# Performance work log

Measured on AMD Instinct MI355X. Metric: run time of the kernel, lower is better.

Reference implementation:

```python
import jax, jax.numpy as jnp
import numpy as np

E = 500_000
NODE_DIM = 128
EDGE_DIM = 128
GLOB_DIM = 64
NUM_GRAPHS = 64
HIDDEN = 4 * EDGE_DIM  # 512
IN_DIM = 2 * NODE_DIM + EDGE_DIM + GLOB_DIM  # 448
EPS = 1e-5


def setup_inputs() -> dict:
    key = jax.random.key(0)
    ks = jax.random.split(key, 12)
    src = jax.random.normal(ks[0], (E, NODE_DIM), dtype=jnp.float32)
    dest = jax.random.normal(ks[1], (E, NODE_DIM), dtype=jnp.float32)
    edge_attr = jax.random.normal(ks[2], (E, EDGE_DIM), dtype=jnp.float32)
    u = jax.random.normal(ks[3], (NUM_GRAPHS, GLOB_DIM), dtype=jnp.float32)
    batch = jnp.sort(jax.random.randint(ks[4], (E,), 0, NUM_GRAPHS, dtype=jnp.int32))
    # MLP params (kaiming-ish scale)
    W1 = jax.random.normal(ks[5], (IN_DIM, HIDDEN), dtype=jnp.float32) / np.sqrt(IN_DIM)
    b1 = jnp.zeros((HIDDEN,), dtype=jnp.float32)
    W2 = jax.random.normal(ks[6], (HIDDEN, EDGE_DIM), dtype=jnp.float32) / np.sqrt(HIDDEN)
    b2 = jnp.zeros((EDGE_DIM,), dtype=jnp.float32)
    # GraphNorm params
    gn_weight = jnp.ones((EDGE_DIM,), dtype=jnp.float32)
    gn_bias = jnp.zeros((EDGE_DIM,), dtype=jnp.float32)
    mean_scale = jnp.ones((EDGE_DIM,), dtype=jnp.float32)
    return {"src": src, "dest": dest, "edge_attr": edge_attr, "u": u, "batch": batch,
            "W1": W1, "b1": b1, "W2": W2, "b2": b2,
            "gn_weight": gn_weight, "gn_bias": gn_bias, "mean_scale": mean_scale}


def _graph_norm(x, batch, weight, bias, mean_scale):
    # per-graph mean
    cnt = jax.ops.segment_sum(jnp.ones((x.shape[0],), x.dtype), batch, num_segments=NUM_GRAPHS)
    cnt = jnp.maximum(cnt, 1.0)[:, None]  # [G,1]
    mean = jax.ops.segment_sum(x, batch, num_segments=NUM_GRAPHS) / cnt  # [G,D]
    out = x - mean[batch] * mean_scale
    var = jax.ops.segment_sum(out * out, batch, num_segments=NUM_GRAPHS) / cnt  # [G,D]
    std = jnp.sqrt(var + EPS)
    return out / std[batch] * weight + bias


def reference(src, dest, edge_attr, u, batch, W1, b1, W2, b2, gn_weight, gn_bias, mean_scale):
    # gather per-graph globals + concat: [E, 2*node+edge+glob]
    h = jnp.concatenate([src, dest, edge_attr, u[batch]], axis=1)
    h = jax.nn.relu(h @ W1 + b1) @ W2 + b2  # [E, edge_dim]
    out = _graph_norm(h + edge_attr, batch, gn_weight, gn_bias, mean_scale)
    return out  # dropout is identity in eval / p=0.0
```

## Files before the change

kernel.cpp:

```cpp
#include <hip/hip_runtime.h>
#include <stdint.h>

#define E_EDGES   500000
#define MBLK      32
#define NBLK      15625
#define EPSV      1e-5f

typedef unsigned short u16;
typedef __attribute__((ext_vector_type(8))) short short8;
typedef __attribute__((ext_vector_type(4))) float f32x4;

__device__ __forceinline__ u16 f2bf(float f) {
  uint32_t u = __float_as_uint(f);
  u += 0x7fffu + ((u >> 16) & 1u);
  return (u16)(u >> 16);
}

__global__ void prep_weights(const float* __restrict__ W1, const float* __restrict__ W2,
                             u16* __restrict__ w1f, u16* __restrict__ w2f) {
  int idx = blockIdx.x * blockDim.x + threadIdx.x;
  if (idx < 32*14*64) {
    int lane = idx & 63; int t = idx >> 6; int k32 = t % 14; int n16 = t / 14;
    int n = n16*16 + (lane & 15); int k0 = k32*32 + (lane >> 4)*8;
    short8 pk;
#pragma unroll
    for (int j = 0; j < 8; ++j) pk[j] = (short)f2bf(W1[(size_t)(k0 + j)*512 + n]);
    *(short8*)&w1f[(size_t)idx * 8] = pk;
  } else if (idx < 32*14*64 + 8*16*64) {
    int i2 = idx - 32*14*64;
    int lane = i2 & 63; int t = i2 >> 6; int k32 = t % 16; int n16 = t / 16;
    int n = n16*16 + (lane & 15); int k0 = k32*32 + (lane >> 4)*8;
    short8 pk;
#pragma unroll
    for (int j = 0; j < 8; ++j) pk[j] = (short)f2bf(W2[(size_t)(k0 + j)*128 + n]);
    *(short8*)&w2f[(size_t)i2 * 8] = pk;
  }
}

#define SWZ16(row, byte) ((byte) ^ (((row) & 7) << 4))

__global__ __launch_bounds__(256, 4)
void fused_kernel(const float* __restrict__ srcp, const float* __restrict__ destp,
                  const float* __restrict__ edgep, const float* __restrict__ up,
                  const int* __restrict__ batch, const float* __restrict__ b1,
                  const float* __restrict__ b2,
                  const u16* __restrict__ w1f, const u16* __restrict__ w2f,
                  float* __restrict__ outp,
                  float* __restrict__ sums0, float* __restrict__ sums2,
                  float* __restrict__ cntsh, int nshard) {
  const int tid  = threadIdx.x;
  const int lane = tid & 63;
  const int w    = tid >> 6;
  const int l15  = lane & 15, l4 = lane >> 4;

  __shared__ __align__(16) u16 lds[32*512];
  char* ldsb = (char*)lds;

  const long grow0 = (long)blockIdx.x * MBLK;

  {
    const int srow = tid >> 3;
    const int c8   = (tid & 7) * 8;
    const long sgrow = grow0 + srow;
    const int  bat = batch[sgrow];
#pragma unroll
    for (int j = 0; j < 7; ++j) {
      const float* sp;
      if (j == 0)      sp = srcp  + sgrow*128 + c8;
      else if (j == 1) sp = srcp  + sgrow*128 + 64 + c8;
      else if (j == 2) sp = destp + sgrow*128 + c8;
      else if (j == 3) sp = destp + sgrow*128 + 64 + c8;
      else if (j == 4) sp = edgep + sgrow*128 + c8;
      else if (j == 5) sp = edgep + sgrow*128 + 64 + c8;
      else             sp = up + (size_t)bat*64 + c8;
      f32x4 t0 = *(const f32x4*)(sp);
      f32x4 t1 = *(const f32x4*)(sp + 4);
      short8 pk;
      pk[0]=(short)f2bf(t0[0]); pk[1]=(short)f2bf(t0[1]);
      pk[2]=(short)f2bf(t0[2]); pk[3]=(short)f2bf(t0[3]);
      pk[4]=(short)f2bf(t1[0]); pk[5]=(short)f2bf(t1[1]);
      pk[6]=(short)f2bf(t1[2]); pk[7]=(short)f2bf(t1[3]);
      *(short8*)(ldsb + srow*896 + SWZ16(srow, (j*64 + c8)*2)) = pk;
    }
  }
  __syncthreads();

  f32x4 acc1[2][8];
#pragma unroll
  for (int mi = 0; mi < 2; ++mi)
#pragma unroll
    for (int nj = 0; nj < 8; ++nj) {
      float bv = b1[w*128 + nj*16 + l15];
      acc1[mi][nj] = (f32x4){bv, bv, bv, bv};
    }

#pragma unroll 2
  for (int k32 = 0; k32 < 14; ++k32) {
    short8 a[2], b[8];
#pragma unroll
    for (int mi = 0; mi < 2; ++mi) {
      int row = mi*16 + l15;
      a[mi] = *(const short8*)(ldsb + row*896 + SWZ16(row, k32*64 + l4*16));
    }
#pragma unroll
    for (int nj = 0; nj < 8; ++nj) {
      int n16 = w*8 + nj;
      b[nj] = *(const short8*)&w1f[((size_t)(n16*14 + k32)*64 + lane)*8];
    }
#pragma unroll
    for (int mi = 0; mi < 2; ++mi)
#pragma unroll
      for (int nj = 0; nj < 8; ++nj)
        acc1[mi][nj] = __builtin_amdgcn_mfma_f32_16x16x32_bf16(a[mi], b[nj], acc1[mi][nj], 0, 0, 0);
  }
  __syncthreads();

#pragma unroll
  for (int nj = 0; nj < 8; ++nj) {
    int n = w*128 + nj*16 + l15;
#pragma unroll
    for (int mi = 0; mi < 2; ++mi)
#pragma unroll
      for (int rr = 0; rr < 4; ++rr) {
        int row = mi*16 + l4*4 + rr;
        *(u16*)(ldsb + row*1024 + SWZ16(row, n*2)) = f2bf(fmaxf(acc1[mi][nj][rr], 0.f));
      }
  }
  __syncthreads();

  const int c4    = tid & 31;
  const int rbase = tid >> 5;
  f32x4 ebuf[4];
#pragma unroll
  for (int p = 0; p < 4; ++p)
    ebuf[p] = *(const f32x4*)(edgep + (grow0 + rbase + p*8)*128 + c4*4);

  f32x4 acc2[2][2];
#pragma unroll
  for (int nj = 0; nj < 2; ++nj) {
    float bv = b2[w*32 + nj*16 + l15];
    acc2[0][nj] = (f32x4){bv, bv, bv, bv};
    acc2[1][nj] = (f32x4){bv, bv, bv, bv};
  }

#pragma unroll 4
  for (int kb = 0; kb < 16; ++kb) {
    short8 a2[2], bf[2];
#pragma unroll
    for (int mi = 0; mi < 2; ++mi) {
      int row = mi*16 + l15;
      a2[mi] = *(const short8*)(ldsb + row*1024 + SWZ16(row, kb*64 + l4*16));
    }
#pragma unroll
    for (int nj = 0; nj < 2; ++nj) {
      int n16 = w*2 + nj;
      bf[nj] = *(const short8*)&w2f[(((size_t)(n16*16 + kb))*64 + lane)*8];
    }
#pragma unroll
    for (int mi = 0; mi < 2; ++mi)
#pragma unroll
      for (int nj = 0; nj < 2; ++nj)
        acc2[mi][nj] = __builtin_amdgcn_mfma_f32_16x16x32_bf16(a2[mi], bf[nj], acc2[mi][nj], 0, 0, 0);
  }
  __syncthreads();

#pragma unroll
  for (int mi = 0; mi < 2; ++mi)
#pragma unroll
    for (int nj = 0; nj < 2; ++nj) {
      int col = w*32 + nj*16 + l15;
#pragma unroll
      for (int rr = 0; rr < 4; ++rr) {
        int row = mi*16 + l4*4 + rr;
        *(float*)(ldsb + row*512 + SWZ16(row, col*4)) = acc2[mi][nj][rr];
      }
    }
  __syncthreads();

  const int g0 = batch[grow0];
  const int g1 = batch[grow0 + MBLK - 1];
  const int sh = blockIdx.x & (nshard - 1);

  if (g0 == g1) {
    f32x4 s = (f32x4){0,0,0,0}, s2 = (f32x4){0,0,0,0};
#pragma unroll
    for (int p = 0; p < 4; ++p) {
      int row = rbase + p*8;
      f32x4 y = *(const f32x4*)(ldsb + row*512 + SWZ16(row, c4*16));
      y = y + ebuf[p];
      *(f32x4*)(outp + (grow0 + row)*128 + c4*4) = y;
      s = s + y; s2 = s2 + y*y;
    }
    int slot = 16384 + (rbase*32 + c4)*32;
    *(f32x4*)(ldsb + slot)      = s;
    *(f32x4*)(ldsb + slot + 16) = s2;
    __syncthreads();
    int c4r = tid >> 3, stat = (tid >> 2) & 1, cq = tid & 3;
    float v = 0.f;
#pragma unroll
    for (int r = 0; r < 8; ++r)
      v += *(const float*)(ldsb + 16384 + (r*32 + c4r)*32 + stat*16 + cq*4);
    float* dst = stat ? sums2 : sums0;
    atomicAdd(&dst[(size_t)sh*8192 + g0*128 + c4r*4 + cq], v);
    if (tid == 0) atomicAdd(&cntsh[sh*64 + g0], (float)MBLK);
  } else {
    f32x4 s = (f32x4){0,0,0,0}, s2 = (f32x4){0,0,0,0};
    float rc = 0.f; int gcur = -1;
#pragma unroll
    for (int p = 0; p < 4; ++p) {
      int row = rbase + p*8;
      int g = batch[grow0 + row];
      if (g != gcur) {
        if (gcur >= 0) {
#pragma unroll
          for (int c = 0; c < 4; ++c) {
            atomicAdd(&sums0[(size_t)sh*8192 + gcur*128 + c4*4 + c], s[c]);
            atomicAdd(&sums2[(size_t)sh*8192 + gcur*128 + c4*4 + c], s2[c]);
          }
          if (c4 == 0) atomicAdd(&cntsh[sh*64 + gcur], rc);
        }
        gcur = g; s = (f32x4){0,0,0,0}; s2 = (f32x4){0,0,0,0}; rc = 0.f;
      }
      f32x4 y = *(const f32x4*)(ldsb + row*512 + SWZ16(row, c4*16));
      y = y + ebuf[p];
      *(f32x4*)(outp + (grow0 + row)*128 + c4*4) = y;
      s = s + y; s2 = s2 + y*y; rc += 1.f;
    }
#pragma unroll
    for (int c = 0; c < 4; ++c) {
      atomicAdd(&sums0[(size_t)sh*8192 + gcur*128 + c4*4 + c], s[c]);
      atomicAdd(&sums2[(size_t)sh*8192 + gcur*128 + c4*4 + c], s2[c]);
    }
    if (c4 == 0) atomicAdd(&cntsh[sh*64 + gcur], rc);
  }
}

__global__ void finalize_kernel(const float* __restrict__ sums0, const float* __restrict__ sums2,
                                const float* __restrict__ cntsh, int nshard,
                                const float* __restrict__ gnw, const float* __restrict__ gnb,
                                const float* __restrict__ ms,
                                float* __restrict__ scale, float* __restrict__ shift) {
  int idx = blockIdx.x*blockDim.x + threadIdx.x;
  if (idx >= 64*128) return;
  int g = idx >> 7, d = idx & 127;
  float s = 0.f, s2 = 0.f, c = 0.f;
  for (int sh = 0; sh < nshard; ++sh) {
    s  += sums0[(size_t)sh*8192 + idx];
    s2 += sums2[(size_t)sh*8192 + idx];
    c  += cntsh[sh*64 + g];
  }
  c = fmaxf(c, 1.0f);
  float mean = s / c;
  float mm = mean * ms[d];
  float var = fmaxf(s2 / c - 2.f*mm*mean + mm*mm, 0.f);
  float sc = gnw[d] / sqrtf(var + EPSV);
  scale[idx] = sc;
  shift[idx] = gnb[d] - mm*sc;
}

__global__ void norm_kernel(float* __restrict__ y, const int* __restrict__ batch,
                            const float* __restrict__ scale, const float* __restrict__ shift) {
  long i = (long)blockIdx.x*blockDim.x + threadIdx.x;
  const long n4 = (long)E_EDGES * 32;
  long stride = (long)gridDim.x*blockDim.x;
  for (; i < n4; i += stride) {
    long row = i >> 5;
    int dq = (int)(i & 31) << 2;
    int g = batch[row];
    f32x4 v = *(f32x4*)(y + i*4);
    f32x4 sc = *(const f32x4*)(scale + g*128 + dq);
    f32x4 sh = *(const f32x4*)(shift + g*128 + dq);
    v = v*sc + sh;
    *(f32x4*)(y + i*4) = v;
  }
}

extern "C" void kernel_launch(void* const* d_in, const int* in_sizes, int n_in,
                              void* d_out, int out_size, void* d_ws, size_t ws_size,
                              hipStream_t stream) {
  const float* srcp  = (const float*)d_in[0];
  const float* destp = (const float*)d_in[1];
  const float* edgep = (const float*)d_in[2];
  const float* up    = (const float*)d_in[3];
  const int*   batch = (const int*)d_in[4];
  const float* W1    = (const float*)d_in[5];
  const float* b1    = (const float*)d_in[6];
  const float* W2    = (const float*)d_in[7];
  const float* b2    = (const float*)d_in[8];
  const float* gnw   = (const float*)d_in[9];
  const float* gnb   = (const float*)d_in[10];
  const float* ms    = (const float*)d_in[11];
  float* outp = (float*)d_out;

  char* ws = (char*)d_ws;
  u16*   w1f   = (u16*)(ws + 0);
  u16*   w2f   = (u16*)(ws + 458752);
  float* scale = (float*)(ws + 589824);
  float* shift = (float*)(ws + 622592);
  float* cntsh = (float*)(ws + 655360);
  int nshard = 32;
  while (nshard > 1 && 663552 + (size_t)nshard*65536 > ws_size) nshard >>= 1;
  float* sums0 = (float*)(ws + 663552);
  float* sums2 = (float*)(ws + 663552 + (size_t)nshard*32768);

  hipMemsetAsync(ws + 655360, 0, 8192 + (size_t)nshard*65536, stream);
  prep_weights<<<dim3(144), dim3(256), 0, stream>>>(W1, W2, w1f, w2f);

  fused_kernel<<<dim3(NBLK), dim3(256), 0, stream>>>(srcp, destp, edgep, up, batch,
                                                     b1, b2, w1f, w2f, outp,
                                                     sums0, sums2, cntsh, nshard);

  finalize_kernel<<<dim3(32), dim3(256), 0, stream>>>(sums0, sums2, cntsh, nshard,
                                                      gnw, gnb, ms, scale, shift);
  norm_kernel<<<dim3(2048), dim3(256), 0, stream>>>(outp, batch, scale, shift);
}
```

Measured before the change: 577.4 us.

## Use library bf16 conversion, full unroll GEMM loops, add MFMA setprio

Replaces the manual round-to-nearest-even bf16 conversion with the HIP library intrinsic and writes the LDS staging as two 8-byte stores instead of one 16-byte packed store. Fully unrolls both GEMM k-loops and wraps the MFMA bursts in s_setprio so the wave issuing matrix ops gets priority over other waves. The goal is less conversion ALU work and better MFMA issue scheduling, at the cost of more code size and register pressure from the full unroll, which could reduce occupancy.

```diff
diff --git a/kernel.cpp b/kernel.cpp
--- a/kernel.cpp
+++ b/kernel.cpp
@@ -1,4 +1,5 @@
 #include <hip/hip_runtime.h>
+#include <hip/hip_bf16.h>
 #include <stdint.h>
 
 #define E_EDGES   500000
@@ -9,11 +10,14 @@
 typedef unsigned short u16;
 typedef __attribute__((ext_vector_type(8))) short short8;
 typedef __attribute__((ext_vector_type(4))) float f32x4;
+typedef __attribute__((ext_vector_type(2))) uint32_t u32x2;
 
 __device__ __forceinline__ u16 f2bf(float f) {
-  uint32_t u = __float_as_uint(f);
-  u += 0x7fffu + ((u >> 16) & 1u);
-  return (u16)(u >> 16);
+  __hip_bfloat16 h = __float2bfloat16(f);
+  return *(u16*)&h;
+}
+__device__ __forceinline__ uint32_t pk2bf(float lo, float hi) {
+  return (uint32_t)f2bf(lo) | ((uint32_t)f2bf(hi) << 16);
 }
 
 __global__ void prep_weights(const float* __restrict__ W1, const float* __restrict__ W2,
@@ -75,26 +79,24 @@
       else             sp = up + (size_t)bat*64 + c8;
       f32x4 t0 = *(const f32x4*)(sp);
       f32x4 t1 = *(const f32x4*)(sp + 4);
-      short8 pk;
-      pk[0]=(short)f2bf(t0[0]); pk[1]=(short)f2bf(t0[1]);
-      pk[2]=(short)f2bf(t0[2]); pk[3]=(short)f2bf(t0[3]);
-      pk[4]=(short)f2bf(t1[0]); pk[5]=(short)f2bf(t1[1]);
-      pk[6]=(short)f2bf(t1[2]); pk[7]=(short)f2bf(t1[3]);
-      *(short8*)(ldsb + srow*896 + SWZ16(srow, (j*64 + c8)*2)) = pk;
+      u32x2 lohi0 = (u32x2){pk2bf(t0[0], t0[1]), pk2bf(t0[2], t0[3])};
+      u32x2 lohi1 = (u32x2){pk2bf(t1[0], t1[1]), pk2bf(t1[2], t1[3])};
+      char* dst = ldsb + srow*896 + SWZ16(srow, (j*64 + c8)*2);
+      *(u32x2*)(dst)     = lohi0;
+      *(u32x2*)(dst + 8) = lohi1;
     }
   }
   __syncthreads();
 
   f32x4 acc1[2][8];
 #pragma unroll
-  for (int mi = 0; mi < 2; ++mi)
-#pragma unroll
-    for (int nj = 0; nj < 8; ++nj) {
-      float bv = b1[w*128 + nj*16 + l15];
-      acc1[mi][nj] = (f32x4){bv, bv, bv, bv};
-    }
-
-#pragma unroll 2
+  for (int nj = 0; nj < 8; ++nj) {
+    float bv = b1[(w*8 + nj)*16 + l15];
+    acc1[0][nj] = (f32x4){bv, bv, bv, bv};
+    acc1[1][nj] = (f32x4){bv, bv, bv, bv};
+  }
+
+#pragma unroll
   for (int k32 = 0; k32 < 14; ++k32) {
     short8 a[2], b[8];
 #pragma unroll
@@ -103,21 +105,21 @@
       a[mi] = *(const short8*)(ldsb + row*896 + SWZ16(row, k32*64 + l4*16));
     }
 #pragma unroll
-    for (int nj = 0; nj < 8; ++nj) {
-      int n16 = w*8 + nj;
-      b[nj] = *(const short8*)&w1f[((size_t)(n16*14 + k32)*64 + lane)*8];
-    }
+    for (int nj = 0; nj < 8; ++nj)
+      b[nj] = *(const short8*)&w1f[((size_t)((w*8 + nj)*14 + k32)*64 + lane)*8];
+    __builtin_amdgcn_s_setprio(1);
 #pragma unroll
     for (int mi = 0; mi < 2; ++mi)
 #pragma unroll
       for (int nj = 0; nj < 8; ++nj)
         acc1[mi][nj] = __builtin_amdgcn_mfma_f32_16x16x32_bf16(a[mi], b[nj], acc1[mi][nj], 0, 0, 0);
+    __builtin_amdgcn_s_setprio(0);
   }
   __syncthreads();
 
 #pragma unroll
   for (int nj = 0; nj < 8; ++nj) {
-    int n = w*128 + nj*16 + l15;
+    int n = (w*8 + nj)*16 + l15;
 #pragma unroll
     for (int mi = 0; mi < 2; ++mi)
 #pragma unroll
@@ -138,37 +140,37 @@
   f32x4 acc2[2][2];
 #pragma unroll
   for (int nj = 0; nj < 2; ++nj) {
-    float bv = b2[w*32 + nj*16 + l15];
+    float bv = b2[(w*2 + nj)*16 + l15];
     acc2[0][nj] = (f32x4){bv, bv, bv, bv};
     acc2[1][nj] = (f32x4){bv, bv, bv, bv};
   }
 
-#pragma unroll 4
+#pragma unroll
   for (int kb = 0; kb < 16; ++kb) {
-    short8 a2[2], bf[2];
+    short8 hb[2], wfr[2];
 #pragma unroll
     for (int mi = 0; mi < 2; ++mi) {
       int row = mi*16 + l15;
-      a2[mi] = *(const short8*)(ldsb + row*1024 + SWZ16(row, kb*64 + l4*16));
-    }
+      hb[mi] = *(const short8*)(ldsb + row*1024 + SWZ16(row, kb*64 + l4*16));
+    }
+#pragma unroll
+    for (int nj = 0; nj < 2; ++nj)
+      wfr[nj] = *(const short8*)&w2f[(((size_t)((w*2 + nj)*16 + kb))*64 + lane)*8];
+    __builtin_amdgcn_s_setprio(1);
+#pragma unroll
+    for (int mi = 0; mi < 2; ++mi)
+#pragma unroll
+      for (int nj = 0; nj < 2; ++nj)
+        acc2[mi][nj] = __builtin_amdgcn_mfma_f32_16x16x32_bf16(hb[mi], wfr[nj], acc2[mi][nj], 0, 0, 0);
+    __builtin_amdgcn_s_setprio(0);
+  }
+  __syncthreads();
+
+#pragma unroll
+  for (int mi = 0; mi < 2; ++mi)
 #pragma unroll
     for (int nj = 0; nj < 2; ++nj) {
-      int n16 = w*2 + nj;
-      bf[nj] = *(const short8*)&w2f[(((size_t)(n16*16 + kb))*64 + lane)*8];
-    }
-#pragma unroll
-    for (int mi = 0; mi < 2; ++mi)
-#pragma unroll
-      for (int nj = 0; nj < 2; ++nj)
-        acc2[mi][nj] = __builtin_amdgcn_mfma_f32_16x16x32_bf16(a2[mi], bf[nj], acc2[mi][nj], 0, 0, 0);
-  }
-  __syncthreads();
-
-#pragma unroll
-  for (int mi = 0; mi < 2; ++mi)
-#pragma unroll
-    for (int nj = 0; nj < 2; ++nj) {
-      int col = w*32 + nj*16 + l15;
+      int col = (w*2 + nj)*16 + l15;
 #pragma unroll
       for (int rr = 0; rr < 4; ++rr) {
         int row = mi*16 + l4*4 + rr;
```

After: 580.7 us. No clear change (+0.6%).
